# Optimization experiments

Measured on AMD Instinct MI355X. Metric: run time of the kernel, lower is better.

The kernel has to match this reference:

```python
import jax, jax.numpy as jnp
import numpy as np

EPS = 1e-5  # nn.BatchNorm1d default eps


def setup_inputs() -> dict:
    key = jax.random.key(0)
    ks = jax.random.split(key, 8)
    N_NODES, N_EDGES = 50000, 800000
    D_NODE, D_EDGE, HID, NCLS = 128, 64, 256, 8
    D_IN = D_EDGE + 2 * D_NODE  # 320
    return {
        "n_feats": jax.random.normal(ks[0], (N_NODES, D_NODE), dtype=jnp.float32),
        "edge_feats": jax.random.normal(ks[1], (N_EDGES, D_EDGE), dtype=jnp.float32),
        "src_idx": jax.random.randint(ks[2], (N_EDGES,), 0, N_NODES, dtype=jnp.int64),
        "dst_idx": jax.random.randint(ks[3], (N_EDGES,), 0, N_NODES, dtype=jnp.int64),
        "W1": jax.random.normal(ks[4], (HID, D_IN), dtype=jnp.float32) * (1.0 / np.sqrt(D_IN)),
        "b1": jnp.zeros((HID,), dtype=jnp.float32),
        "gamma": jnp.ones((HID,), dtype=jnp.float32),
        "beta": jnp.zeros((HID,), dtype=jnp.float32),
        "W2": jax.random.normal(ks[5], (NCLS, HID), dtype=jnp.float32) * (1.0 / np.sqrt(HID)),
        "b2": jnp.zeros((NCLS,), dtype=jnp.float32),
    }


def reference(n_feats, edge_feats, src_idx, dst_idx, W1, b1, gamma, beta, W2, b2):
    # gather-concat: [E, d_edge + 2*d_node]
    h = jnp.concatenate([edge_feats, n_feats[src_idx], n_feats[dst_idx]], axis=1)
    # Linear 1
    z = jnp.einsum("ei,hi->eh", h, W1) + b1
    # BatchNorm1d in training mode: batch mean / biased variance over edges
    mu = jnp.mean(z, axis=0)
    var = jnp.mean(jnp.square(z - mu), axis=0)
    zn = (z - mu) * jax.lax.rsqrt(var + EPS) * gamma + beta
    # Linear 2 + LogSoftmax(dim=1)
    logits = jnp.einsum("eh,ch->ec", zn, W2) + b2
    return jax.nn.log_softmax(logits, axis=1)
```

## Files before the change

### kernel.cpp

```cpp
#include <hip/hip_runtime.h>
#include <hip/hip_bf16.h>


#define N_EDGES 800000
#define N_NODES 50000

typedef __attribute__((ext_vector_type(8))) short short8;
typedef __attribute__((ext_vector_type(4))) float f32x4;

#define WS_SUM   0
#define WS_SQ    16384
#define WS_CVEC  32768
#define WS_FLAG  32832
#define WS_MBIG  33280
#define WS_MB    43520
#define WS_MF    45568
#define WS_W1B   55808
#define WS_PS    262144
#define WS_PD    2097152
#define WS_NFB   4194304
#define WS_FAST_NEED (4u << 20)
#define WS_BIG_NEED  16994304u

__device__ __forceinline__ ushort f2bf(float f) {
    union { float f; unsigned int u; } x; x.f = f;
    unsigned int r = x.u + 0x7FFFu + ((x.u >> 16) & 1u);
    return (ushort)(r >> 16);
}
__device__ __forceinline__ short8 cvt8(const float* __restrict__ p) {
    short8 r;
    #pragma unroll
    for (int i = 0; i < 8; i++) r[i] = (short)f2bf(p[i]);
    return r;
}
__device__ __forceinline__ short8 cvtpair(uint4 a, uint4 b) {
    unsigned int v[8] = {a.x, a.y, a.z, a.w, b.x, b.y, b.z, b.w};
    short8 r;
    #pragma unroll
    for (int i = 0; i < 8; i++) {
        unsigned int u = v[i];
        unsigned int rr = u + 0x7FFFu + ((u >> 16) & 1u);
        r[i] = (short)(rr >> 16);
    }
    return r;
}

__device__ __forceinline__ int aidx(int s, int r, int c) {
    return ((s * 64 + r) * 4 + (c ^ ((r >> 1) & 3))) * 8;
}

__global__ void detect_kernel(const int* __restrict__ src,
                              const int* __restrict__ dst, int* flag) {
    int t = threadIdx.x;
    int v = src[2 * t + 1] | dst[2 * t + 1];
    #pragma unroll
    for (int o = 32; o >= 1; o >>= 1) v |= __shfl_xor(v, o);
    if (t == 0) *flag = (v == 0) ? 1 : 0;
}

__global__ __launch_bounds__(256) void prep_kernel(const float* __restrict__ W1,
                                                   ushort* __restrict__ W1b) {
    const int i = (blockIdx.x * 256 + threadIdx.x) * 4;
    const float4 v = *(const float4*)(W1 + i);
    ushort4 o;
    o.x = f2bf(v.x); o.y = f2bf(v.y); o.z = f2bf(v.z); o.w = f2bf(v.w);
    *(ushort4*)(W1b + i) = o;
}

__global__ __launch_bounds__(256) void prep_all_kernel(
    const float* __restrict__ nf, const float* __restrict__ W1,
    const int* __restrict__ src, const int* __restrict__ dst,
    ushort* __restrict__ nfb, ushort* __restrict__ W1b,
    float* __restrict__ zreg, int* __restrict__ flag)
{
    const int t = threadIdx.x;
    const int b = blockIdx.x;
    if (b < 3125) {
        const long i = (long)b * 2048 + t * 8;
        const float4 v0 = *(const float4*)(nf + i);
        const float4 v1 = *(const float4*)(nf + i + 4);
        short8 o;
        o[0] = (short)f2bf(v0.x); o[1] = (short)f2bf(v0.y);
        o[2] = (short)f2bf(v0.z); o[3] = (short)f2bf(v0.w);
        o[4] = (short)f2bf(v1.x); o[5] = (short)f2bf(v1.y);
        o[6] = (short)f2bf(v1.z); o[7] = (short)f2bf(v1.w);
        *(short8*)(nfb + i) = o;
    } else if (b < 3205) {
        const int i = (b - 3125) * 1024 + t * 4;
        const float4 v = *(const float4*)(W1 + i);
        ushort4 o;
        o.x = f2bf(v.x); o.y = f2bf(v.y); o.z = f2bf(v.z); o.w = f2bf(v.w);
        *(ushort4*)(W1b + i) = o;
    } else {
        for (int i = t; i < 8320; i += 256) zreg[i] = 0.f;
        __syncthreads();
        if (t < 64) {
            int v = src[2 * t + 1] | dst[2 * t + 1];
            #pragma unroll
            for (int o = 32; o >= 1; o >>= 1) v |= __shfl_xor(v, o);
            if (t == 0) *flag = (v == 0) ? 1 : 0;
        }
    }
}

template <bool NFB>
__global__ __launch_bounds__(256) void gemm1_stats_kernel(
    const float* __restrict__ nf, const ushort* __restrict__ nfb,
    const float* __restrict__ ef,
    const int* __restrict__ src, const int* __restrict__ dst,
    const ushort* __restrict__ W1b, const int* __restrict__ flag,
    float* __restrict__ g_sum, float* __restrict__ g_sq)
{
    __shared__ ushort a_lds[10 * 64 * 32];

    const int t    = threadIdx.x;
    const int lane = t & 63;
    const int wave = t >> 6;
    const int quad = lane >> 4;
    const int l15  = lane & 15;

    const int wide = *flag;
    const int r = t >> 2, chunk = t & 3;
    const long e  = (long)blockIdx.x * 64 + r;
    const int si = src[e << wide], di = dst[e << wide];
    const float* pe = ef + e * 64 + chunk * 8;

    uint4 pe0[2], pe1[2];
    pe0[0] = *(const uint4*)pe;        pe0[1] = *(const uint4*)(pe + 4);
    pe1[0] = *(const uint4*)(pe + 32); pe1[1] = *(const uint4*)(pe + 36);

    const ushort* wbase = W1b + (wave * 64 + l15) * 320 + quad * 8;
    short8 bpre[2][4];
    #pragma unroll
    for (int in = 0; in < 4; in++)
        bpre[0][in] = *(const short8*)(wbase + in * 16 * 320);
    #pragma unroll
    for (int in = 0; in < 4; in++)
        bpre[1][in] = *(const short8*)(wbase + in * 16 * 320 + 32);

    if constexpr (NFB) {
        const ushort* psb = nfb + (long)si * 128 + chunk * 8;
        const ushort* pdb = nfb + (long)di * 128 + chunk * 8;
        short8 g[8];
        #pragma unroll
        for (int i = 0; i < 4; i++) g[i]     = *(const short8*)(psb + i * 32);
        #pragma unroll
        for (int i = 0; i < 4; i++) g[4 + i] = *(const short8*)(pdb + i * 32);
        *(short8*)&a_lds[aidx(0, r, chunk)] = cvtpair(pe0[0], pe0[1]);
        *(short8*)&a_lds[aidx(1, r, chunk)] = cvtpair(pe1[0], pe1[1]);
        #pragma unroll
        for (int i = 0; i < 8; i++)
            *(short8*)&a_lds[aidx(2 + i, r, chunk)] = g[i];
    } else {
        const float* ps = nf + (long)si * 128 + chunk * 8;
        const float* pd = nf + (long)di * 128 + chunk * 8;
        uint4 pn[16];
        #pragma unroll
        for (int i = 0; i < 4; i++) {
            pn[i * 2]     = *(const uint4*)(ps + i * 32);
            pn[i * 2 + 1] = *(const uint4*)(ps + i * 32 + 4);
        }
        #pragma unroll
        for (int i = 0; i < 4; i++) {
            pn[8 + i * 2]     = *(const uint4*)(pd + i * 32);
            pn[8 + i * 2 + 1] = *(const uint4*)(pd + i * 32 + 4);
        }
        *(short8*)&a_lds[aidx(0, r, chunk)] = cvtpair(pe0[0], pe0[1]);
        *(short8*)&a_lds[aidx(1, r, chunk)] = cvtpair(pe1[0], pe1[1]);
        #pragma unroll
        for (int i = 0; i < 8; i++)
            *(short8*)&a_lds[aidx(2 + i, r, chunk)] =
                cvtpair(pn[i * 2], pn[i * 2 + 1]);
    }
    __syncthreads();

    f32x4 acc[4][4];
    #pragma unroll
    for (int a = 0; a < 4; a++)
        #pragma unroll
        for (int b = 0; b < 4; b++) acc[a][b] = (f32x4){0.f, 0.f, 0.f, 0.f};

    short8 acur[4], anext[4];
    #pragma unroll
    for (int mb = 0; mb < 4; mb++)
        acur[mb] = *(const short8*)&a_lds[aidx(0, mb * 16 + l15, quad)];

    #pragma unroll
    for (int ks = 0; ks < 10; ks++) {
        short8 bcur[4];
        #pragma unroll
        for (int in = 0; in < 4; in++) bcur[in] = bpre[ks & 1][in];
        if (ks < 8) {
            #pragma unroll
            for (int in = 0; in < 4; in++)
                bpre[ks & 1][in] =
                    *(const short8*)(wbase + in * 16 * 320 + (ks + 2) * 32);
        }
        if (ks < 9) {
            #pragma unroll
            for (int mb = 0; mb < 4; mb++)
                anext[mb] = *(const short8*)
                    &a_lds[aidx(ks + 1, mb * 16 + l15, quad)];
        }
        __builtin_amdgcn_s_setprio(1);
        #pragma unroll
        for (int mb = 0; mb < 4; mb++)
            #pragma unroll
            for (int in = 0; in < 4; in++)
                acc[mb][in] = __builtin_amdgcn_mfma_f32_16x16x32_bf16(
                    acur[mb], bcur[in], acc[mb][in], 0, 0, 0);
        __builtin_amdgcn_s_setprio(0);
        #pragma unroll
        for (int mb = 0; mb < 4; mb++) acur[mb] = anext[mb];
    }

    const int slot = blockIdx.x & 15;
    #pragma unroll
    for (int in = 0; in < 4; in++) {
        const int col = wave * 64 + in * 16 + l15;
        float s = 0.f, q = 0.f;
        #pragma unroll
        for (int mb = 0; mb < 4; mb++)
            #pragma unroll
            for (int j = 0; j < 4; j++) {
                float v = acc[mb][in][j];
                s += v; q += v * v;
            }
        s += __shfl_xor(s, 16); s += __shfl_xor(s, 32);
        q += __shfl_xor(q, 16); q += __shfl_xor(q, 32);
        if (quad == 0) {
            atomicAdd(&g_sum[slot * 256 + col], s);
            atomicAdd(&g_sq[slot * 256 + col], q);
        }
    }
}

__global__ __launch_bounds__(256) void fold_kernel(
    const float* __restrict__ gamma, const float* __restrict__ beta,
    const float* __restrict__ W1, const float* __restrict__ b1,
    const float* __restrict__ W2, const float* __restrict__ b2,
    const float* __restrict__ g_sum, const float* __restrict__ g_sq,
    ushort* __restrict__ Mbig, ushort* __restrict__ Mb,
    float* __restrict__ Mf, float* __restrict__ Cvec)
{
    __shared__ float a_sh[256][8];
    __shared__ float red[8];
    __shared__ float mk_sh[64][8];
    const int t = threadIdx.x;

    float ssum = 0.f, ssq = 0.f;
    #pragma unroll
    for (int s = 0; s < 16; s++) {
        ssum += g_sum[s * 256 + t];
        ssq  += g_sq[s * 256 + t];
    }
    const float invE   = 1.0f / (float)N_EDGES;
    const float mu_acc = ssum * invE;
    float var = ssq * invE - mu_acc * mu_acc;
    var = fmaxf(var, 0.f);
    const float b1v = b1[t];
    const float mu  = mu_acc + b1v;
    const float g   = gamma[t] * rsqrtf(var + 1e-5f);
    const float sh  = b1v * g + beta[t] - mu * g;

    if (t < 8) red[t] = 0.f;
    ((float*)mk_sh)[t] = 0.f;
    ((float*)mk_sh)[t + 256] = 0.f;
    __syncthreads();
    #pragma unroll
    for (int c = 0; c < 8; c++) {
        const float w = W2[c * 256 + t];
        a_sh[t][c] = w * g;
        if (blockIdx.x == 0) atomicAdd(&red[c], w * sh);
    }
    __syncthreads();

    const int k  = blockIdx.x * 64 + (t & 63);
    const int q4 = t >> 6;
    float m[8] = {0.f, 0.f, 0.f, 0.f, 0.f, 0.f, 0.f, 0.f};
    for (int hh = q4 * 64; hh < q4 * 64 + 64; hh++) {
        const float w1 = W1[hh * 320 + k];
        #pragma unroll
        for (int c = 0; c < 8; c++) m[c] += a_sh[hh][c] * w1;
    }
    #pragma unroll
    for (int c = 0; c < 8; c++) atomicAdd(&mk_sh[t & 63][c], m[c]);
    __syncthreads();

    if (t < 64) {
        const int kk = blockIdx.x * 64 + t;
        #pragma unroll
        for (int c = 0; c < 8; c++) {
            const float mv = mk_sh[t][c];
            Mf[c * 320 + kk]   = mv;
            Mbig[c * 320 + kk] = f2bf(mv);
            if (kk < 64) Mb[c * 64 + kk] = f2bf(mv);
        }
        #pragma unroll
        for (int c = 8; c < 16; c++) {
            Mbig[c * 320 + kk] = 0;
            if (kk < 64) Mb[c * 64 + kk] = 0;
        }
    }
    if (blockIdx.x == 0) {
        if (t < 8)       Cvec[t] = b2[t] + red[t];
        else if (t < 16) Cvec[t] = 0.f;
    }
}

__global__ __launch_bounds__(256) void fold_nodeproj_kernel(
    const float* __restrict__ gamma, const float* __restrict__ beta,
    const float* __restrict__ W1, const float* __restrict__ b1,
    const float* __restrict__ W2, const float* __restrict__ b2,
    const float* __restrict__ g_sum, const float* __restrict__ g_sq,
    const float* __restrict__ nf, ushort* __restrict__ Mb,
    float* __restrict__ Cvec, float* __restrict__ Ps, float* __restrict__ Pd)
{
    __shared__ float a_sh[256][8];
    __shared__ float red[8];
    __shared__ float Ms[8][128];
    __shared__ float Md[8][128];
    const int t = threadIdx.x;

    float ssum = 0.f, ssq = 0.f;
    #pragma unroll
    for (int s = 0; s < 16; s++) {
        ssum += g_sum[s * 256 + t];
        ssq  += g_sq[s * 256 + t];
    }
    const float invE   = 1.0f / (float)N_EDGES;
    const float mu_acc = ssum * invE;
    float var = ssq * invE - mu_acc * mu_acc;
    var = fmaxf(var, 0.f);
    const float b1v = b1[t];
    const float mu  = mu_acc + b1v;
    const float g   = gamma[t] * rsqrtf(var + 1e-5f);
    const float sh  = b1v * g + beta[t] - mu * g;

    if (t < 8) red[t] = 0.f;
    __syncthreads();
    #pragma unroll
    for (int c = 0; c < 8; c++) {
        const float w = W2[c * 256 + t];
        a_sh[t][c] = w * g;
        if (blockIdx.x == 0) atomicAdd(&red[c], w * sh);
    }
    __syncthreads();

    float m[8] = {0.f, 0.f, 0.f, 0.f, 0.f, 0.f, 0.f, 0.f};
    for (int hh = 0; hh < 256; hh++) {
        const float w1 = W1[hh * 320 + 64 + t];
        #pragma unroll
        for (int c = 0; c < 8; c++) m[c] += a_sh[hh][c] * w1;
    }
    #pragma unroll
    for (int c = 0; c < 8; c++) {
        if (t < 128) Ms[c][t] = m[c];
        else         Md[c][t - 128] = m[c];
    }
    if (blockIdx.x == 0) {
        if (t < 64) {
            float mm[8] = {0.f, 0.f, 0.f, 0.f, 0.f, 0.f, 0.f, 0.f};
            for (int hh = 0; hh < 256; hh++) {
                const float w1 = W1[hh * 320 + t];
                #pragma unroll
                for (int c = 0; c < 8; c++) mm[c] += a_sh[hh][c] * w1;
            }
            #pragma unroll
            for (int c = 0; c < 8; c++)  Mb[c * 64 + t] = f2bf(mm[c]);
            #pragma unroll
            for (int c = 8; c < 16; c++) Mb[c * 64 + t] = 0;
        }
        if (t < 8)       Cvec[t] = b2[t] + red[t];
        else if (t < 16) Cvec[t] = 0.f;
    }
    __syncthreads();

    const int n = blockIdx.x * 256 + t;
    if (n >= N_NODES) return;
    float as[8] = {0,0,0,0,0,0,0,0}, ad[8] = {0,0,0,0,0,0,0,0};
    for (int k = 0; k < 128; k += 4) {
        const float4 v = *(const float4*)(nf + (long)n * 128 + k);
        #pragma unroll
        for (int c = 0; c < 8; c++) {
            const float4 ms = *(const float4*)&Ms[c][k];
            const float4 md = *(const float4*)&Md[c][k];
            as[c] += v.x * ms.x + v.y * ms.y + v.z * ms.z + v.w * ms.w;
            ad[c] += v.x * md.x + v.y * md.y + v.z * md.z + v.w * md.w;
        }
    }
    #pragma unroll
    for (int c = 0; c < 8; c++) {
        Ps[n * 8 + c] = as[c];
        Pd[n * 8 + c] = ad[c];
    }
}

__global__ __launch_bounds__(256) void nodeproj_kernel(
    const float* __restrict__ nf, const float* __restrict__ Mf,
    float* __restrict__ Ps, float* __restrict__ Pd)
{
    __shared__ float Ms[8][128];
    __shared__ float Md[8][128];
    const int t = threadIdx.x;
    #pragma unroll
    for (int i = 0; i < 4; i++) {
        const int f = t + i * 256;
        Ms[f >> 7][f & 127] = Mf[(f >> 7) * 320 + 64  + (f & 127)];
        Md[f >> 7][f & 127] = Mf[(f >> 7) * 320 + 192 + (f & 127)];
    }
    __syncthreads();
    const int n = blockIdx.x * 256 + t;
    if (n >= N_NODES) return;
    float as[8] = {0,0,0,0,0,0,0,0}, ad[8] = {0,0,0,0,0,0,0,0};
    for (int k = 0; k < 128; k += 4) {
        const float4 v = *(const float4*)(nf + (long)n * 128 + k);
        #pragma unroll
        for (int c = 0; c < 8; c++) {
            const float4 ms = *(const float4*)&Ms[c][k];
            const float4 md = *(const float4*)&Md[c][k];
            as[c] += v.x * ms.x + v.y * ms.y + v.z * ms.z + v.w * ms.w;
            ad[c] += v.x * md.x + v.y * md.y + v.z * md.z + v.w * md.w;
        }
    }
    #pragma unroll
    for (int c = 0; c < 8; c++) {
        Ps[n * 8 + c] = as[c];
        Pd[n * 8 + c] = ad[c];
    }
}

__global__ __launch_bounds__(256) void edge_out_kernel(
    const float* __restrict__ ef, const int* __restrict__ src,
    const int* __restrict__ dst, const int* __restrict__ flag,
    const ushort* __restrict__ Mb, const float* __restrict__ Ps,
    const float* __restrict__ Pd, const float* __restrict__ Cvec,
    float* __restrict__ out)
{
    __shared__ float pv_sh[4][64][9];
    const int t    = threadIdx.x;
    const int lane = t & 63;
    const int wave = t >> 6;
    const int quad = lane >> 4;
    const int l15  = lane & 15;
    const int wide = *flag;
    const long eb  = (long)blockIdx.x * 256 + wave * 64;

    const long ei = (eb + lane) << wide;
    const int sidx = src[ei], didx = dst[ei];
    const float4 s0 = *(const float4*)(Ps + sidx * 8);
    const float4 s1 = *(const float4*)(Ps + sidx * 8 + 4);
    const float4 d0 = *(const float4*)(Pd + didx * 8);
    const float4 d1 = *(const float4*)(Pd + didx * 8 + 4);

    uint4 ea[4][2], eb4[4][2];
    #pragma unroll
    for (int mb = 0; mb < 4; mb++)
        #pragma unroll
        for (int ks = 0; ks < 2; ks++) {
            const float* p = ef + (eb + mb * 16 + l15) * 64 + ks * 32 + quad * 8;
            ea[mb][ks]  = *(const uint4*)p;
            eb4[mb][ks] = *(const uint4*)(p + 4);
        }

    pv_sh[wave][lane][0] = s0.x + d0.x;
    pv_sh[wave][lane][1] = s0.y + d0.y;
    pv_sh[wave][lane][2] = s0.z + d0.z;
    pv_sh[wave][lane][3] = s0.w + d0.w;
    pv_sh[wave][lane][4] = s1.x + d1.x;
    pv_sh[wave][lane][5] = s1.y + d1.y;
    pv_sh[wave][lane][6] = s1.z + d1.z;
    pv_sh[wave][lane][7] = s1.w + d1.w;

    f32x4 acc[4];
    #pragma unroll
    for (int mb = 0; mb < 4; mb++) acc[mb] = (f32x4){0.f, 0.f, 0.f, 0.f};

    const ushort* bbase = Mb + l15 * 64 + quad * 8;
    #pragma unroll
    for (int ks = 0; ks < 2; ks++) {
        short8 bfr = *(const short8*)(bbase + ks * 32);
        #pragma unroll
        for (int mb = 0; mb < 4; mb++)
            acc[mb] = __builtin_amdgcn_mfma_f32_16x16x32_bf16(
                cvtpair(ea[mb][ks], eb4[mb][ks]), bfr, acc[mb], 0, 0, 0);
    }

    const float bv = Cvec[l15];
    #pragma unroll
    for (int mb = 0; mb < 4; mb++) {
        #pragma unroll
        for (int j = 0; j < 4; j++) {
            const int er = mb * 16 + quad * 4 + j;
            const float pv = (l15 < 8) ? pv_sh[wave][er][l15] : 0.f;
            float x = acc[mb][j] + bv + pv;
            float m = x;
            m = fmaxf(m, __shfl_xor(m, 1));
            m = fmaxf(m, __shfl_xor(m, 2));
            m = fmaxf(m, __shfl_xor(m, 4));
            float sx = __expf(x - m);
            sx += __shfl_xor(sx, 1);
            sx += __shfl_xor(sx, 2);
            sx += __shfl_xor(sx, 4);
            const float o = x - m - __logf(sx);
            if (l15 < 8) out[(eb + er) * 8 + l15] = o;
        }
    }
}

__global__ __launch_bounds__(256) void out_kernel(
    const float* __restrict__ nf, const float* __restrict__ ef,
    const int* __restrict__ src, const int* __restrict__ dst,
    const int* __restrict__ flag, const ushort* __restrict__ M,
    const float* __restrict__ Cvec, float* __restrict__ out)
{
    const int t    = threadIdx.x;
    const int lane = t & 63;
    const int wave = t >> 6;
    const int quad = lane >> 4;
    const int l15  = lane & 15;
    const int wide = *flag;
    const long eb  = (long)blockIdx.x * 256 + wave * 64;

    const float* pe[4]; const float* ps[4]; const float* pd[4];
    #pragma unroll
    for (int mb = 0; mb < 4; mb++) {
        const long e  = eb + mb * 16 + l15;
        const int si = src[e << wide], di = dst[e << wide];
        pe[mb] = ef + e * 64;
        ps[mb] = nf + (long)si * 128;
        pd[mb] = nf + (long)di * 128;
    }
    f32x4 acc[4];
    #pragma unroll
    for (int mb = 0; mb < 4; mb++) acc[mb] = (f32x4){0.f, 0.f, 0.f, 0.f};
    const ushort* bbase = M + l15 * 320 + quad * 8;
    #pragma unroll
    for (int ks = 0; ks < 10; ks++) {
        const int k0 = ks * 32;
        short8 bfr = *(const short8*)(bbase + k0);
        const int koff = k0 + quad * 8;
        #pragma unroll
        for (int mb = 0; mb < 4; mb++) {
            const float* p = (ks < 2) ? (pe[mb] + koff)
                           : (ks < 6) ? (ps[mb] + (koff - 64))
                                      : (pd[mb] + (koff - 192));
            acc[mb] = __builtin_amdgcn_mfma_f32_16x16x32_bf16(
                cvt8(p), bfr, acc[mb], 0, 0, 0);
        }
    }
    const float bv = Cvec[l15];
    #pragma unroll
    for (int mb = 0; mb < 4; mb++)
        #pragma unroll
        for (int j = 0; j < 4; j++) {
            float x = acc[mb][j] + bv;
            float m = x;
            m = fmaxf(m, __shfl_xor(m, 1));
            m = fmaxf(m, __shfl_xor(m, 2));
            m = fmaxf(m, __shfl_xor(m, 4));
            float sx = __expf(x - m);
            sx += __shfl_xor(sx, 1);
            sx += __shfl_xor(sx, 2);
            sx += __shfl_xor(sx, 4);
            const float o = x - m - __logf(sx);
            if (l15 < 8)
                out[(eb + mb * 16 + quad * 4 + j) * 8 + l15] = o;
        }
}

extern "C" void kernel_launch(void* const* d_in, const int* in_sizes, int n_in,
                              void* d_out, int out_size, void* d_ws, size_t ws_size,
                              hipStream_t stream) {
    const float* nf    = (const float*)d_in[0];
    const float* ef    = (const float*)d_in[1];
    const int*   src   = (const int*)d_in[2];
    const int*   dst   = (const int*)d_in[3];
    const float* W1    = (const float*)d_in[4];
    const float* b1    = (const float*)d_in[5];
    const float* gamma = (const float*)d_in[6];
    const float* beta  = (const float*)d_in[7];
    const float* W2    = (const float*)d_in[8];
    const float* b2    = (const float*)d_in[9];

    char*   ws    = (char*)d_ws;
    float*  g_sum = (float*)(ws + WS_SUM);
    float*  g_sq  = (float*)(ws + WS_SQ);
    float*  Cvec  = (float*)(ws + WS_CVEC);
    int*    flag  = (int*)(ws + WS_FLAG);
    ushort* Mbig  = (ushort*)(ws + WS_MBIG);
    ushort* Mb    = (ushort*)(ws + WS_MB);
    float*  Mf    = (float*)(ws + WS_MF);
    ushort* W1b   = (ushort*)(ws + WS_W1B);
    float*  Ps    = (float*)(ws + WS_PS);
    float*  Pd    = (float*)(ws + WS_PD);
    ushort* nfb   = (ushort*)(ws + WS_NFB);
    float*  out   = (float*)d_out;

    const bool fast = ws_size >= (size_t)WS_FAST_NEED;
    const bool big  = ws_size >= (size_t)WS_BIG_NEED;

    if (big) {
        prep_all_kernel<<<3206, 256, 0, stream>>>(nf, W1, src, dst, nfb, W1b,
                                                  (float*)ws, flag);
        gemm1_stats_kernel<true><<<N_EDGES / 64, 256, 0, stream>>>(
            nf, nfb, ef, src, dst, W1b, flag, g_sum, g_sq);
        fold_nodeproj_kernel<<<(N_NODES + 255) / 256, 256, 0, stream>>>(
            gamma, beta, W1, b1, W2, b2, g_sum, g_sq, nf, Mb, Cvec, Ps, Pd);
        edge_out_kernel<<<N_EDGES / 256, 256, 0, stream>>>(ef, src, dst, flag,
                                                           Mb, Ps, Pd, Cvec, out);
    } else {
        hipMemsetAsync(ws, 0, 33280, stream);
        detect_kernel<<<1, 64, 0, stream>>>(src, dst, flag);
        prep_kernel<<<80, 256, 0, stream>>>(W1, W1b);
        gemm1_stats_kernel<false><<<N_EDGES / 64, 256, 0, stream>>>(
            nf, nfb, ef, src, dst, W1b, flag, g_sum, g_sq);
        fold_kernel<<<5, 256, 0, stream>>>(gamma, beta, W1, b1, W2, b2,
                                           g_sum, g_sq, Mbig, Mb, Mf, Cvec);
        if (fast) {
            nodeproj_kernel<<<(N_NODES + 255) / 256, 256, 0, stream>>>(nf, Mf, Ps, Pd);
            edge_out_kernel<<<N_EDGES / 256, 256, 0, stream>>>(ef, src, dst, flag,
                                                               Mb, Ps, Pd, Cvec, out);
        } else {
            out_kernel<<<N_EDGES / 256, 256, 0, stream>>>(nf, ef, src, dst, flag,
                                                          Mbig, Cvec, out);
        }
    }
}
```

Measured before the change: 623.1 us.

## Enlarge GEMM1 tile to 128 edges with 8 waves, rework edge softmax epilogue

The gemm1_stats kernel now processes 128 edges per block with 512 threads. Each of its 8 waves covers 32 output columns across 8 row blocks, which halves the block count and roughly doubles LDS use. The B fragments rotate through a three-slot prefetch buffer, and A fragments are read from LDS inside the MFMA loop instead of being double-buffered. The edge_out epilogue stages accumulators in LDS so that each lane computes a full 8-class log-softmax and writes it with vectorized stores, replacing the shuffle reductions. Several scalar loops in the fold and nodeproj kernels get unroll pragmas.

```diff
diff --git a/kernel.cpp b/kernel.cpp
--- a/kernel.cpp
+++ b/kernel.cpp
@@ -46,7 +46,7 @@
 }
 
 __device__ __forceinline__ int aidx(int s, int r, int c) {
-    return ((s * 64 + r) * 4 + (c ^ ((r >> 1) & 3))) * 8;
+    return ((s * 128 + r) * 4 + (c ^ ((r >> 1) & 3))) * 8;
 }
 
 __global__ void detect_kernel(const int* __restrict__ src,
@@ -104,14 +104,14 @@
 }
 
 template <bool NFB>
-__global__ __launch_bounds__(256) void gemm1_stats_kernel(
+__global__ __launch_bounds__(512, 4) void gemm1_stats_kernel(
     const float* __restrict__ nf, const ushort* __restrict__ nfb,
     const float* __restrict__ ef,
     const int* __restrict__ src, const int* __restrict__ dst,
     const ushort* __restrict__ W1b, const int* __restrict__ flag,
     float* __restrict__ g_sum, float* __restrict__ g_sq)
 {
-    __shared__ ushort a_lds[10 * 64 * 32];
+    __shared__ ushort a_lds[10 * 128 * 32];
 
     const int t    = threadIdx.x;
     const int lane = t & 63;
@@ -120,22 +120,27 @@
     const int l15  = lane & 15;
 
     const int wide = *flag;
-    const int r = t >> 2, chunk = t & 3;
-    const long e  = (long)blockIdx.x * 64 + r;
+    const int r     = t >> 2;
+    const int chunk = t & 3;
+    const long e   = (long)blockIdx.x * 128 + r;
     const int si = src[e << wide], di = dst[e << wide];
-    const float* pe = ef + e * 64 + chunk * 8;
-
-    uint4 pe0[2], pe1[2];
-    pe0[0] = *(const uint4*)pe;        pe0[1] = *(const uint4*)(pe + 4);
-    pe1[0] = *(const uint4*)(pe + 32); pe1[1] = *(const uint4*)(pe + 36);
-
-    const ushort* wbase = W1b + (wave * 64 + l15) * 320 + quad * 8;
-    short8 bpre[2][4];
-    #pragma unroll
-    for (int in = 0; in < 4; in++)
+    const float* pe = ef + e * 64;
+
+    uint4 efu[2][2];
+    #pragma unroll
+    for (int s = 0; s < 2; s++) {
+        const float* p = pe + s * 32 + chunk * 8;
+        efu[s][0] = *(const uint4*)p;
+        efu[s][1] = *(const uint4*)(p + 4);
+    }
+
+    const ushort* wbase = W1b + (wave * 32 + l15) * 320 + quad * 8;
+    short8 bpre[3][2];
+    #pragma unroll
+    for (int in = 0; in < 2; in++)
         bpre[0][in] = *(const short8*)(wbase + in * 16 * 320);
     #pragma unroll
-    for (int in = 0; in < 4; in++)
+    for (int in = 0; in < 2; in++)
         bpre[1][in] = *(const short8*)(wbase + in * 16 * 320 + 32);
 
     if constexpr (NFB) {
@@ -146,8 +151,9 @@
         for (int i = 0; i < 4; i++) g[i]     = *(const short8*)(psb + i * 32);
         #pragma unroll
         for (int i = 0; i < 4; i++) g[4 + i] = *(const short8*)(pdb + i * 32);
-        *(short8*)&a_lds[aidx(0, r, chunk)] = cvtpair(pe0[0], pe0[1]);
-        *(short8*)&a_lds[aidx(1, r, chunk)] = cvtpair(pe1[0], pe1[1]);
+        #pragma unroll
+        for (int s = 0; s < 2; s++)
+            *(short8*)&a_lds[aidx(s, r, chunk)] = cvtpair(efu[s][0], efu[s][1]);
         #pragma unroll
         for (int i = 0; i < 8; i++)
             *(short8*)&a_lds[aidx(2 + i, r, chunk)] = g[i];
@@ -165,8 +171,9 @@
             pn[8 + i * 2]     = *(const uint4*)(pd + i * 32);
             pn[8 + i * 2 + 1] = *(const uint4*)(pd + i * 32 + 4);
         }
-        *(short8*)&a_lds[aidx(0, r, chunk)] = cvtpair(pe0[0], pe0[1]);
-        *(short8*)&a_lds[aidx(1, r, chunk)] = cvtpair(pe1[0], pe1[1]);
+        #pragma unroll
+        for (int s = 0; s < 2; s++)
+            *(short8*)&a_lds[aidx(s, r, chunk)] = cvtpair(efu[s][0], efu[s][1]);
         #pragma unroll
         for (int i = 0; i < 8; i++)
             *(short8*)&a_lds[aidx(2 + i, r, chunk)] =
@@ -174,53 +181,41 @@
     }
     __syncthreads();
 
-    f32x4 acc[4][4];
-    #pragma unroll
-    for (int a = 0; a < 4; a++)
-        #pragma unroll
-        for (int b = 0; b < 4; b++) acc[a][b] = (f32x4){0.f, 0.f, 0.f, 0.f};
-
-    short8 acur[4], anext[4];
-    #pragma unroll
-    for (int mb = 0; mb < 4; mb++)
-        acur[mb] = *(const short8*)&a_lds[aidx(0, mb * 16 + l15, quad)];
+    f32x4 acc[8][2];
+    #pragma unroll
+    for (int mb = 0; mb < 8; mb++)
+        #pragma unroll
+        for (int in = 0; in < 2; in++)
+            acc[mb][in] = (f32x4){0.f, 0.f, 0.f, 0.f};
 
     #pragma unroll
     for (int ks = 0; ks < 10; ks++) {
-        short8 bcur[4];
-        #pragma unroll
-        for (int in = 0; in < 4; in++) bcur[in] = bpre[ks & 1][in];
         if (ks < 8) {
             #pragma unroll
-            for (int in = 0; in < 4; in++)
-                bpre[ks & 1][in] =
+            for (int in = 0; in < 2; in++)
+                bpre[(ks + 2) % 3][in] =
                     *(const short8*)(wbase + in * 16 * 320 + (ks + 2) * 32);
         }
-        if (ks < 9) {
+        __builtin_amdgcn_s_setprio(1);
+        #pragma unroll
+        for (int mb = 0; mb < 8; mb++) {
+            short8 afr = *(const short8*)
+                &a_lds[aidx(ks, mb * 16 + l15, quad)];
             #pragma unroll
-            for (int mb = 0; mb < 4; mb++)
-                anext[mb] = *(const short8*)
-                    &a_lds[aidx(ks + 1, mb * 16 + l15, quad)];
-        }
-        __builtin_amdgcn_s_setprio(1);
-        #pragma unroll
-        for (int mb = 0; mb < 4; mb++)
-            #pragma unroll
-            for (int in = 0; in < 4; in++)
+            for (int in = 0; in < 2; in++)
                 acc[mb][in] = __builtin_amdgcn_mfma_f32_16x16x32_bf16(
-                    acur[mb], bcur[in], acc[mb][in], 0, 0, 0);
+                    afr, bpre[ks % 3][in], acc[mb][in], 0, 0, 0);
+        }
         __builtin_amdgcn_s_setprio(0);
-        #pragma unroll
-        for (int mb = 0; mb < 4; mb++) acur[mb] = anext[mb];
     }
 
     const int slot = blockIdx.x & 15;
     #pragma unroll
-    for (int in = 0; in < 4; in++) {
-        const int col = wave * 64 + in * 16 + l15;
+    for (int in = 0; in < 2; in++) {
+        const int col = wave * 32 + in * 16 + l15;
         float s = 0.f, q = 0.f;
         #pragma unroll
-        for (int mb = 0; mb < 4; mb++)
+        for (int mb = 0; mb < 8; mb++)
             #pragma unroll
             for (int j = 0; j < 4; j++) {
                 float v = acc[mb][in][j];
@@ -278,6 +273,7 @@
     const int k  = blockIdx.x * 64 + (t & 63);
     const int q4 = t >> 6;
     float m[8] = {0.f, 0.f, 0.f, 0.f, 0.f, 0.f, 0.f, 0.f};
+    #pragma unroll 8
     for (int hh = q4 * 64; hh < q4 * 64 + 64; hh++) {
         const float w1 = W1[hh * 320 + k];
         #pragma unroll
@@ -348,6 +344,7 @@
     __syncthreads();
 
     float m[8] = {0.f, 0.f, 0.f, 0.f, 0.f, 0.f, 0.f, 0.f};
+    #pragma unroll 8
     for (int hh = 0; hh < 256; hh++) {
         const float w1 = W1[hh * 320 + 64 + t];
         #pragma unroll
@@ -361,6 +358,7 @@
     if (blockIdx.x == 0) {
         if (t < 64) {
             float mm[8] = {0.f, 0.f, 0.f, 0.f, 0.f, 0.f, 0.f, 0.f};
+            #pragma unroll 8
             for (int hh = 0; hh < 256; hh++) {
                 const float w1 = W1[hh * 320 + t];
                 #pragma unroll
@@ -379,6 +377,7 @@
     const int n = blockIdx.x * 256 + t;
     if (n >= N_NODES) return;
     float as[8] = {0,0,0,0,0,0,0,0}, ad[8] = {0,0,0,0,0,0,0,0};
+    #pragma unroll 4
     for (int k = 0; k < 128; k += 4) {
         const float4 v = *(const float4*)(nf + (long)n * 128 + k);
         #pragma unroll
@@ -413,6 +412,7 @@
     const int n = blockIdx.x * 256 + t;
     if (n >= N_NODES) return;
     float as[8] = {0,0,0,0,0,0,0,0}, ad[8] = {0,0,0,0,0,0,0,0};
+    #pragma unroll 4
     for (int k = 0; k < 128; k += 4) {
         const float4 v = *(const float4*)(nf + (long)n * 128 + k);
         #pragma unroll
@@ -437,7 +437,7 @@
     const float* __restrict__ Pd, const float* __restrict__ Cvec,
     float* __restrict__ out)
 {
-    __shared__ float pv_sh[4][64][9];
+    __shared__ float x_sh[4][64][16];
     const int t    = threadIdx.x;
     const int lane = t & 63;
     const int wave = t >> 6;
@@ -452,6 +452,8 @@
     const float4 s1 = *(const float4*)(Ps + sidx * 8 + 4);
     const float4 d0 = *(const float4*)(Pd + didx * 8);
     const float4 d1 = *(const float4*)(Pd + didx * 8 + 4);
+    const float4 c0 = *(const float4*)(Cvec);
+    const float4 c1 = *(const float4*)(Cvec + 4);
 
     uint4 ea[4][2], eb4[4][2];
     #pragma unroll
@@ -463,15 +465,6 @@
             eb4[mb][ks] = *(const uint4*)(p + 4);
         }
 
-    pv_sh[wave][lane][0] = s0.x + d0.x;
-    pv_sh[wave][lane][1] = s0.y + d0.y;
-    pv_sh[wave][lane][2] = s0.z + d0.z;
-    pv_sh[wave][lane][3] = s0.w + d0.w;
-    pv_sh[wave][lane][4] = s1.x + d1.x;
-    pv_sh[wave][lane][5] = s1.y + d1.y;
-    pv_sh[wave][lane][6] = s1.z + d1.z;
-    pv_sh[wave][lane][7] = s1.w + d1.w;
-
     f32x4 acc[4];
     #pragma unroll
     for (int mb = 0; mb < 4; mb++) acc[mb] = (f32x4){0.f, 0.f, 0.f, 0.f};
@@ -486,26 +479,37 @@
                 cvtpair(ea[mb][ks], eb4[mb][ks]), bfr, acc[mb], 0, 0, 0);
     }
 
-    const float bv = Cvec[l15];
-    #pragma unroll
-    for (int mb = 0; mb < 4; mb++) {
-        #pragma unroll
-        for (int j = 0; j < 4; j++) {
-            const int er = mb * 16 + quad * 4 + j;
-            const float pv = (l15 < 8) ? pv_sh[wave][er][l15] : 0.f;
-            float x = acc[mb][j] + bv + pv;
-            float m = x;
-            m = fmaxf(m, __shfl_xor(m, 1));
-            m = fmaxf(m, __shfl_xor(m, 2));
-            m = fmaxf(m, __shfl_xor(m, 4));
-            float sx = __expf(x - m);
-            sx += __shfl_xor(sx, 1);
-            sx += __shfl_xor(sx, 2);
-            sx += __shfl_xor(sx, 4);
-            const float o = x - m - __logf(sx);
-            if (l15 < 8) out[(eb + er) * 8 + l15] = o;
-        }
-    }
+    #pragma unroll
+    for (int mb = 0; mb < 4; mb++)
+        #pragma unroll
+        for (int j = 0; j < 4; j++)
+            x_sh[wave][mb * 16 + quad * 4 + j][l15] = acc[mb][j];
+    __syncthreads();
+
+    const float4 xa = *(const float4*)&x_sh[wave][lane][0];
+    const float4 xb = *(const float4*)&x_sh[wave][lane][4];
+
+    float x0 = xa.x + c0.x + s0.x + d0.x;
+    float x1 = xa.y + c0.y + s0.y + d0.y;
+    float x2 = xa.z + c0.z + s0.z + d0.z;
+    float x3 = xa.w + c0.w + s0.w + d0.w;
+    float x4 = xb.x + c1.x + s1.x + d1.x;
+    float x5 = xb.y + c1.y + s1.y + d1.y;
+    float x6 = xb.z + c1.z + s1.z + d1.z;
+    float x7 = xb.w + c1.w + s1.w + d1.w;
+
+    float m = fmaxf(fmaxf(fmaxf(x0, x1), fmaxf(x2, x3)),
+                    fmaxf(fmaxf(x4, x5), fmaxf(x6, x7)));
+    float sx = __expf(x0 - m) + __expf(x1 - m) + __expf(x2 - m) +
+               __expf(x3 - m) + __expf(x4 - m) + __expf(x5 - m) +
+               __expf(x6 - m) + __expf(x7 - m);
+    const float l = m + __logf(sx);
+
+    float* po = out + (eb + lane) * 8;
+    float4 o0 = {x0 - l, x1 - l, x2 - l, x3 - l};
+    float4 o1 = {x4 - l, x5 - l, x6 - l, x7 - l};
+    *(float4*)po       = o0;
+    *(float4*)(po + 4) = o1;
 }
 
 __global__ __launch_bounds__(256) void out_kernel(
@@ -603,7 +607,7 @@
     if (big) {
         prep_all_kernel<<<3206, 256, 0, stream>>>(nf, W1, src, dst, nfb, W1b,
                                                   (float*)ws, flag);
-        gemm1_stats_kernel<true><<<N_EDGES / 64, 256, 0, stream>>>(
+        gemm1_stats_kernel<true><<<N_EDGES / 128, 512, 0, stream>>>(
             nf, nfb, ef, src, dst, W1b, flag, g_sum, g_sq);
         fold_nodeproj_kernel<<<(N_NODES + 255) / 256, 256, 0, stream>>>(
             gamma, beta, W1, b1, W2, b2, g_sum, g_sq, nf, Mb, Cvec, Ps, Pd);
@@ -613,7 +617,7 @@
         hipMemsetAsync(ws, 0, 33280, stream);
         detect_kernel<<<1, 64, 0, stream>>>(src, dst, flag);
         prep_kernel<<<80, 256, 0, stream>>>(W1, W1b);
-        gemm1_stats_kernel<false><<<N_EDGES / 64, 256, 0, stream>>>(
+        gemm1_stats_kernel<false><<<N_EDGES / 128, 512, 0, stream>>>(
             nf, nfb, ef, src, dst, W1b, flag, g_sum, g_sq);
         fold_kernel<<<5, 256, 0, stream>>>(gamma, beta, W1, b1, W2, b2,
                                            g_sum, g_sq, Mbig, Mb, Mf, Cvec);
```

Result: faster. 516.9 us (-17.0%).
